# Kernel tuning notes

Hardware: AMD Instinct MI355X
Metric: run time of the kernel (lower is better)

Reference implementation:

```python
import jax, jax.numpy as jnp
import numpy as np

THETA0 = 3.0
THETA = 5.0
R = 5  # window radius == theta; the sdf is clipped to [-theta, theta], so distances beyond R are saturated

# all integer offsets within Euclidean radius THETA (78 of them)
_OFFSETS = [(dy, dx, float(np.hypot(dy, dx)))
            for dy in range(-R, R + 1) for dx in range(-R, R + 1)
            if np.hypot(dy, dx) <= THETA]


def _capped_edt(target_set):
    """target_set: bool [B,H,W]. Min Euclidean distance from each pixel to a True
    pixel, capped at THETA (exact for all values that survive the later clip)."""
    B, H, W = target_set.shape
    pad = jnp.pad(target_set, ((0, 0), (R, R), (R, R)), constant_values=False)
    d = jnp.full((B, H, W), THETA, dtype=jnp.float32)
    for dy, dx, dist in _OFFSETS:
        win = pad[:, R + dy:R + dy + H, R + dx:R + dx + W]
        d = jnp.minimum(d, jnp.where(win, jnp.float32(dist), jnp.float32(THETA)))
    return d


def _compute_sdf(mask):
    """mask: float [B,H,W]. Mirrors BoundaryLoss.compute_sdf:
    sdf_pos = edt(1-mask) = dist to nearest pixel where mask==1 (zeros of 1-mask)
    sdf_neg = edt(mask)   = dist to nearest pixel where mask==0
    (the `boundary` tensor in the torch code is computed but never used)."""
    sdf_pos = _capped_edt(mask == 1.0)
    sdf_neg = _capped_edt(mask == 0.0)
    sdf = jnp.clip(sdf_pos - sdf_neg, -THETA, THETA) / THETA
    empty = jnp.sum(mask, axis=(1, 2)) == 0.0  # per-batch empty-mask branch -> theta0
    return jnp.where(empty[:, None, None], jnp.float32(THETA0), sdf)


def _boundary_loss(pred, target):
    p = jax.nn.softmax(pred, axis=1)  # [B,C,H,W]
    C = pred.shape[1]
    loss = jnp.float32(0.0)
    for c in range(C):  # small fixed class count
        pred_sdf = _compute_sdf(p[:, c])
        tgt_sdf = _compute_sdf((target == c).astype(jnp.float32))
        loss = loss + jnp.mean(jnp.abs(pred_sdf - tgt_sdf))  # F.l1_loss, mean
    return loss / C


def setup_inputs() -> dict:
    key = jax.random.key(0)
    k1, k2 = jax.random.split(key)
    pred = jax.random.normal(k1, (16, 4, 512, 512), dtype=jnp.float32)
    target = jax.random.randint(k2, (16, 512, 512), 0, 4, dtype=jnp.int32)
    return {"pred": pred, "target": target}


def reference(pred, target):
    return _boundary_loss(pred, target)
```

## Files before the change

kernel.cpp:

```cpp
#include <hip/hip_runtime.h>
#include <stdint.h>

#define BB 16
#define CC 4
#define HH 512
#define WW 512
#define NWORDS 8
#define HW (HH * WW)

#define OFF_ROW   1024
#define OFF_TGT   262144
#define BOARD_BYTES (CC * BB * HH * NWORDS * 8)

__global__ void build_bits(const int* __restrict__ tgt,
                           const float* __restrict__ pred,
                           uint64_t* __restrict__ tgtb,
                           uint64_t* __restrict__ ppos,
                           uint64_t* __restrict__ pneg,
                           unsigned* __restrict__ rowsum,
                           float* __restrict__ out) {
    __shared__ unsigned srow[CC][8];
    int row = blockIdx.x;
    int b = row >> 9, y = row & (HH - 1);
    int x = threadIdx.x;
    if (row == 0 && x == 0) out[0] = 0.0f;

    int t = tgt[((size_t)(b * HH + y)) * WW + x];
    size_t i0 = (((size_t)b * CC) * HH + y) * (size_t)WW + x;
    float a0 = pred[i0];
    float a1 = pred[i0 + (size_t)HW];
    float a2 = pred[i0 + 2 * (size_t)HW];
    float a3 = pred[i0 + 3 * (size_t)HW];
    float m = fmaxf(fmaxf(a0, a1), fmaxf(a2, a3));
    float e0 = expf(a0 - m), e1 = expf(a1 - m), e2 = expf(a2 - m), e3 = expf(a3 - m);
    float s = (e0 + e1) + (e2 + e3);
    float p0 = e0 / s, p1 = e1 / s, p2 = e2 / s, p3 = e3 / s;

    int wv = x >> 6;
    bool l0 = (x & 63) == 0;
#define EMIT(cidx, pv)                                                        \
    {                                                                         \
        uint64_t mt = __ballot(t == (cidx));                                  \
        uint64_t mp = __ballot((pv) == 1.0f);                                 \
        uint64_t mn = __ballot((pv) == 0.0f);                                 \
        if (l0) {                                                             \
            size_t o = (((size_t)(cidx) * BB + b) * HH + y) * NWORDS + wv;    \
            tgtb[o] = mt;                                                     \
            ppos[o] = mp;                                                     \
            pneg[o] = mn;                                                     \
            srow[cidx][wv] = (mt != 0ull ? 1u : 0u) | (mp != 0ull ? 2u : 0u)  \
                           | (mn != 0ull ? 4u : 0u) | (mn == ~0ull ? 8u : 0u);\
        }                                                                     \
    }
    EMIT(0, p0)
    EMIT(1, p1)
    EMIT(2, p2)
    EMIT(3, p3)
#undef EMIT
    __syncthreads();
    if (x < CC) {
        unsigned o = 0u, a = 8u;
#pragma unroll
        for (int i = 0; i < 8; ++i) { o |= srow[x][i]; a &= srow[x][i]; }
        rowsum[((size_t)x * BB + b) * HH + y] = (o & 7u) | a;
    }
}

__device__ __forceinline__ constexpr int lev_idx(int d2) {
    return d2==0?0: d2==1?1: d2==2?2: d2==4?3: d2==5?4: d2==8?5: d2==9?6:
           d2==10?7: d2==13?8: d2==16?9: d2==17?10: d2==18?11: d2==20?12: 13;
}

__device__ __forceinline__ unsigned win11(const uint64_t* row10, int idx, int p) {
    uint64_t w;
    if (p < 64) {
        w = (row10[idx] >> p) | (row10[idx + 1] << (64 - p));
    } else {
        int q = p - 64;
        uint64_t M = row10[idx + 1];
        w = q ? ((M >> q) | (row10[idx + 2] << (64 - q))) : M;
    }
    return (unsigned)w & 0x7FFu;
}

__device__ __forceinline__ void upd(int& mind2, unsigned wbits, int dy2) {
    if (wbits) {
        unsigned hi = wbits >> 5;
        unsigned lo = wbits & 31u;
        int mdx = 6;
        if (hi) mdx = __ffs(hi) - 1;
        if (lo) {
            int m2 = 5 - (31 - __clz(lo));
            mdx = min(mdx, m2);
        }
        int cand = dy2 + mdx * mdx;
        mind2 = min(mind2, cand);
    }
}

__launch_bounds__(512)
__global__ void edt_main(const uint64_t* __restrict__ tgtb,
                         const uint64_t* __restrict__ pposb,
                         const uint64_t* __restrict__ pnegb,
                         const unsigned* __restrict__ rowsum,
                         float* __restrict__ out) {
    __shared__ uint64_t shm[74 * 8];
    __shared__ float wsum[8];
    __shared__ unsigned sflag[8];
    int tile = blockIdx.x & 7;
    int cb   = blockIdx.x >> 3;
    int y0   = tile * 64;
    const float INV_N = 1.0f / 16777216.0f;

    {
        unsigned rs = rowsum[(size_t)cb * HH + threadIdx.x];
        uint64_t bT = __ballot((rs & 1u) != 0u);
        uint64_t bP = __ballot((rs & 2u) != 0u);
        uint64_t bN = __ballot((rs & 4u) != 0u);
        uint64_t bAllNot = __ballot((rs & 8u) == 0u);
        if ((threadIdx.x & 63) == 0)
            sflag[threadIdx.x >> 6] = (bT ? 1u : 0u) | (bP ? 2u : 0u)
                                    | (bN ? 4u : 0u) | (bAllNot ? 8u : 0u);
        __syncthreads();
        if (threadIdx.x == 0) {
            unsigned o = 0u;
#pragma unroll
            for (int i = 0; i < 8; ++i) o |= sflag[i];
            sflag[0] = o;
        }
        __syncthreads();
    }
    unsigned F = sflag[0];
    bool present  = (F & 1u) != 0u;
    bool anyppos  = (F & 2u) != 0u;
    bool anypneg  = (F & 4u) != 0u;
    bool prednz   = (F & 8u) != 0u;
    bool fast     = !anyppos && !anypneg;
    __syncthreads();

    if (fast) {
        if (!present) {
            if (tile == 0 && threadIdx.x == 0)
                atomicAdd(out, 3.0f * (float)HW * INV_N);
            return;
        }
        uint64_t (*sT)[8] = (uint64_t (*)[8])shm;
        const uint64_t* board = tgtb + (size_t)cb * HH * NWORDS;
        for (int t = threadIdx.x; t < 74 * 8; t += 512) {
            int r = t >> 3, w = t & 7;
            int yy = y0 + r - 5;
            sT[r][w] = (yy >= 0 && yy < HH) ? board[(size_t)yy * NWORDS + w] : 0ull;
        }
        __syncthreads();

        int tr = threadIdx.x >> 3;
        int w  = threadIdx.x & 7;
        int y  = y0 + tr;

        uint64_t DT[14], DC[14];
#pragma unroll
        for (int k = 0; k < 14; ++k) { DT[k] = 0ull; DC[k] = 0ull; }

#pragma unroll
        for (int dy = -5; dy <= 5; ++dy) {
            int yy = y + dy;
            if (yy < 0 || yy >= HH) continue;
            const int ady  = dy < 0 ? -dy : dy;
            const int maxs = (ady == 0) ? 5 : (ady <= 3) ? 4 : (ady == 4) ? 3 : 0;
            int ly = tr + 5 + dy;
            uint64_t Cw = sT[ly][w];
            uint64_t Lw = (w > 0) ? sT[ly][w - 1] : 0ull;
            uint64_t Rw = (w < 7) ? sT[ly][w + 1] : 0ull;
            uint64_t Cc = ~Cw;
            uint64_t Lc = (w > 0) ? ~Lw : 0ull;
            uint64_t Rc = (w < 7) ? ~Rw : 0ull;
            uint64_t UT = Cw, UC = Cc;
            DT[lev_idx(ady * ady)] |= UT;
            DC[lev_idx(ady * ady)] |= UC;
#pragma unroll
            for (int s = 1; s <= 5; ++s) {
                if (s > maxs) break;
                UT |= (Cw >> s) | (Rw << (64 - s)) | (Cw << s) | (Lw >> (64 - s));
                UC |= (Cc >> s) | (Rc << (64 - s)) | (Cc << s) | (Lc >> (64 - s));
                const int li = lev_idx(ady * ady + s * s);
                DT[li] |= UT;
                DC[li] |= UC;
            }
        }

        const float dist[14] = {0.f, 1.f, 1.41421356f, 2.f, 2.23606798f,
            2.82842712f, 3.f, 3.16227766f, 3.60555128f, 4.f, 4.12310563f,
            4.24264069f, 4.47213595f, 5.f};
        uint64_t covT = 0ull, covC = 0ull;
        float s = 0.f;
#pragma unroll
        for (int k = 0; k < 14; ++k) {
            uint64_t nT = DT[k] & ~covT;
            uint64_t nC = DC[k] & ~covC;
            s += dist[k] * (float)(__popcll(nT) + __popcll(nC));
            covT |= DT[k];
            covC |= DC[k];
        }
        s += 5.f * (float)(__popcll(~covT) + __popcll(~covC));

        for (int o = 32; o > 0; o >>= 1) s += __shfl_down(s, o, 64);
        if ((threadIdx.x & 63) == 0) wsum[threadIdx.x >> 6] = s;
        __syncthreads();
        if (threadIdx.x == 0) {
            float tot = 0.f;
#pragma unroll
            for (int i = 0; i < 8; ++i) tot += wsum[i];
            atomicAdd(out, tot * 0.2f * INV_N);
        }
        return;
    }

    uint64_t (*sh)[11][10] = (uint64_t (*)[11][10])shm;
    int x = threadIdx.x;
    int idx = x >> 6, off = x & 63, p = off + 59;
    int b = cb & (BB - 1);
    int c = cb >> 4;

    unsigned vmask = 0x7FFu;
    if (x < 5) vmask &= (0x7FFu << (5 - x)) & 0x7FFu;
    if (x > WW - 6) vmask &= 0x7FFu >> (x - (WW - 6));

    float vsum = 0.f;
    for (int yy = 0; yy < 64; ++yy) {
        int y = y0 + yy;
        __syncthreads();
        for (int t = threadIdx.x; t < 330; t += 512) {
            int m = t / 110;
            int rem = t - m * 110;
            int r = rem / 10;
            int wi = rem - r * 10;
            int rowy = y + r - 5;
            uint64_t v = 0;
            if (wi >= 1 && wi <= 8 && rowy >= 0 && rowy < HH) {
                const uint64_t* src = (m == 0) ? tgtb : (m == 1) ? pposb : pnegb;
                v = src[(((size_t)c * BB + b) * HH + rowy) * NWORDS + (wi - 1)];
            }
            sh[m][r][wi] = v;
        }
        __syncthreads();

        int tp = 26, tn = 26, qp = 26, qn = 26;
#pragma unroll
        for (int dy = -5; dy <= 5; ++dy) {
            int ady = dy < 0 ? -dy : dy;
            unsigned allowed = (ady == 0) ? 0x7FFu
                             : (ady <= 3) ? 0x3FEu
                             : (ady == 4) ? 0x1FCu
                                          : 0x020u;
            int dy2 = dy * dy;
            int r = dy + 5;
            unsigned wt  = win11(&sh[0][r][0], idx, p);
            unsigned wpp = win11(&sh[1][r][0], idx, p);
            unsigned wpn = win11(&sh[2][r][0], idx, p);
            upd(tp, wt & allowed, dy2);
            upd(tn, (~wt) & vmask & allowed, dy2);
            upd(qp, wpp & allowed, dy2);
            upd(qn, wpn & allowed, dy2);
        }

        float dtp = (tp <= 25) ? sqrtf((float)tp) : 5.0f;
        float dtn = (tn <= 25) ? sqrtf((float)tn) : 5.0f;
        float dqp = (qp <= 25) ? sqrtf((float)qp) : 5.0f;
        float dqn = (qn <= 25) ? sqrtf((float)qn) : 5.0f;

        float td = fminf(fmaxf(dtp - dtn, -5.0f), 5.0f) / 5.0f;
        float qd = fminf(fmaxf(dqp - dqn, -5.0f), 5.0f) / 5.0f;
        float tsdf = present ? td : 3.0f;
        float psdf = prednz ? qd : 3.0f;
        vsum += fabsf(psdf - tsdf);
    }

    for (int o2 = 32; o2 > 0; o2 >>= 1) vsum += __shfl_down(vsum, o2, 64);
    if (off == 0) wsum[idx] = vsum;
    __syncthreads();
    if (threadIdx.x == 0) {
        float s = 0.f;
#pragma unroll
        for (int i = 0; i < 8; ++i) s += wsum[i];
        atomicAdd(out, s * INV_N);
    }
}

extern "C" void kernel_launch(void* const* d_in, const int* in_sizes, int n_in,
                              void* d_out, int out_size, void* d_ws, size_t ws_size,
                              hipStream_t stream) {
    const float* pred  = (const float*)d_in[0];
    const int* target  = (const int*)d_in[1];
    float* out = (float*)d_out;

    char* ws = (char*)d_ws;
    unsigned* rowsum = (unsigned*)(ws + OFF_ROW);
    uint64_t* tgtb   = (uint64_t*)(ws + OFF_TGT);
    uint64_t* pposb  = (uint64_t*)(ws + OFF_TGT + (size_t)BOARD_BYTES);
    uint64_t* pnegb  = (uint64_t*)(ws + OFF_TGT + 2 * (size_t)BOARD_BYTES);

    hipLaunchKernelGGL(build_bits, dim3(BB * HH), dim3(512), 0, stream,
                       target, pred, tgtb, pposb, pnegb, rowsum, out);
    hipLaunchKernelGGL(edt_main, dim3(CC * BB * 8), dim3(512), 0, stream,
                       tgtb, pposb, pnegb, rowsum, out);
}
```

Before: 125.4 us.

## Vectorize bit-board build, skip softmax when no saturation possible, trim EDT radius

The build kernel now processes four rows per block with int4/float4 loads, packs per-class bits via shuffles into 16-bit stores, and skips the exp/divide softmax entirely for a wavefront unless some pixel's logit range reaches 15, where a probability could round to exactly 0 or 1. Per-row flags for all four classes are packed into one word, replacing the per-class rowsum array. In the fast EDT path, the radius-5 level is dropped and the halo shrinks to 4 rows, using a hand-unrolled per-dy table, because uncovered pixels already default to distance 5. The logit-range threshold is a conservative numerical argument rather than an exact test, which is the main correctness risk.

```diff
diff --git a/kernel.cpp b/kernel.cpp
--- a/kernel.cpp
+++ b/kernel.cpp
@@ -12,63 +12,107 @@
 #define OFF_TGT   262144
 #define BOARD_BYTES (CC * BB * HH * NWORDS * 8)
 
+__launch_bounds__(512)
 __global__ void build_bits(const int* __restrict__ tgt,
                            const float* __restrict__ pred,
                            uint64_t* __restrict__ tgtb,
                            uint64_t* __restrict__ ppos,
                            uint64_t* __restrict__ pneg,
-                           unsigned* __restrict__ rowsum,
+                           unsigned* __restrict__ flags32,
                            float* __restrict__ out) {
-    __shared__ unsigned srow[CC][8];
-    int row = blockIdx.x;
+    __shared__ unsigned sfl[4][2];
+    int t = threadIdx.x;
+    int r = t >> 7;
+    int j = t & 127;
+    int row = blockIdx.x * 4 + r;
     int b = row >> 9, y = row & (HH - 1);
-    int x = threadIdx.x;
-    if (row == 0 && x == 0) out[0] = 0.0f;
-
-    int t = tgt[((size_t)(b * HH + y)) * WW + x];
-    size_t i0 = (((size_t)b * CC) * HH + y) * (size_t)WW + x;
-    float a0 = pred[i0];
-    float a1 = pred[i0 + (size_t)HW];
-    float a2 = pred[i0 + 2 * (size_t)HW];
-    float a3 = pred[i0 + 3 * (size_t)HW];
-    float m = fmaxf(fmaxf(a0, a1), fmaxf(a2, a3));
-    float e0 = expf(a0 - m), e1 = expf(a1 - m), e2 = expf(a2 - m), e3 = expf(a3 - m);
-    float s = (e0 + e1) + (e2 + e3);
-    float p0 = e0 / s, p1 = e1 / s, p2 = e2 / s, p3 = e3 / s;
-
-    int wv = x >> 6;
-    bool l0 = (x & 63) == 0;
-#define EMIT(cidx, pv)                                                        \
-    {                                                                         \
-        uint64_t mt = __ballot(t == (cidx));                                  \
-        uint64_t mp = __ballot((pv) == 1.0f);                                 \
-        uint64_t mn = __ballot((pv) == 0.0f);                                 \
-        if (l0) {                                                             \
-            size_t o = (((size_t)(cidx) * BB + b) * HH + y) * NWORDS + wv;    \
-            tgtb[o] = mt;                                                     \
-            ppos[o] = mp;                                                     \
-            pneg[o] = mn;                                                     \
-            srow[cidx][wv] = (mt != 0ull ? 1u : 0u) | (mp != 0ull ? 2u : 0u)  \
-                           | (mn != 0ull ? 4u : 0u) | (mn == ~0ull ? 8u : 0u);\
-        }                                                                     \
-    }
-    EMIT(0, p0)
-    EMIT(1, p1)
-    EMIT(2, p2)
-    EMIT(3, p3)
-#undef EMIT
+    if (blockIdx.x == 0 && t == 0) out[0] = 0.0f;
+
+    const int4* tg4 = reinterpret_cast<const int4*>(tgt);
+    int4 tv = tg4[(size_t)row * 128 + j];
+
+    float pa[4][4];
+    const float4* pr4 = reinterpret_cast<const float4*>(pred);
+#pragma unroll
+    for (int c = 0; c < 4; ++c) {
+        float4 v = pr4[((size_t)(b * 4 + c) * HH + y) * 128 + j];
+        pa[c][0] = v.x; pa[c][1] = v.y; pa[c][2] = v.z; pa[c][3] = v.w;
+    }
+
+    bool anyhard = false;
+#pragma unroll
+    for (int k = 0; k < 4; ++k) {
+        float mx = fmaxf(fmaxf(pa[0][k], pa[1][k]), fmaxf(pa[2][k], pa[3][k]));
+        float mn = fminf(fminf(pa[0][k], pa[1][k]), fminf(pa[2][k], pa[3][k]));
+        anyhard |= (mx - mn >= 15.0f);
+    }
+    uint64_t hard = __ballot(anyhard);
+
+    unsigned tn[4], ppn[4] = {0u, 0u, 0u, 0u}, pnn[4] = {0u, 0u, 0u, 0u};
+#pragma unroll
+    for (int c = 0; c < 4; ++c)
+        tn[c] = (unsigned)(tv.x == c) | ((unsigned)(tv.y == c) << 1)
+              | ((unsigned)(tv.z == c) << 2) | ((unsigned)(tv.w == c) << 3);
+
+    if (hard) {
+#pragma unroll
+        for (int k = 0; k < 4; ++k) {
+            float mx = fmaxf(fmaxf(pa[0][k], pa[1][k]), fmaxf(pa[2][k], pa[3][k]));
+            float e[4], s = 0.f;
+#pragma unroll
+            for (int c = 0; c < 4; ++c) { e[c] = expf(pa[c][k] - mx); s += e[c]; }
+#pragma unroll
+            for (int c = 0; c < 4; ++c) {
+                float p = e[c] / s;
+                ppn[c] |= (unsigned)(p == 1.0f) << k;
+                pnn[c] |= (unsigned)(p == 0.0f) << k;
+            }
+        }
+    }
+
+    unsigned fl = 0u;
+#pragma unroll
+    for (int c = 0; c < 4; ++c) {
+        unsigned f = (tn[c] ? 1u : 0u) | (ppn[c] ? 2u : 0u) | (pnn[c] ? 4u : 0u)
+                   | ((pnn[c] != 0xFu) ? 8u : 0u);
+        fl |= f << (4 * c);
+    }
+#pragma unroll
+    for (int o = 1; o < 64; o <<= 1) fl |= __shfl_xor(fl, o, 64);
+    if ((t & 63) == 0) sfl[r][(t >> 6) & 1] = fl;
+
+    unsigned short* t16 = reinterpret_cast<unsigned short*>(tgtb);
+    unsigned short* p16 = reinterpret_cast<unsigned short*>(ppos);
+    unsigned short* n16 = reinterpret_cast<unsigned short*>(pneg);
+#pragma unroll
+    for (int c = 0; c < 4; ++c) {
+        size_t base16 = ((size_t)(c * BB + b) * HH + y) * (NWORDS * 4);
+        unsigned v = tn[c];
+        v |= __shfl_down(v, 1, 64) << 4;
+        v |= __shfl_down(v, 2, 64) << 8;
+        if ((j & 3) == 0) t16[base16 + (j >> 2)] = (unsigned short)v;
+        if (hard) {
+            unsigned vp = ppn[c];
+            vp |= __shfl_down(vp, 1, 64) << 4;
+            vp |= __shfl_down(vp, 2, 64) << 8;
+            unsigned vn = pnn[c];
+            vn |= __shfl_down(vn, 1, 64) << 4;
+            vn |= __shfl_down(vn, 2, 64) << 8;
+            if ((j & 3) == 0) {
+                p16[base16 + (j >> 2)] = (unsigned short)vp;
+                n16[base16 + (j >> 2)] = (unsigned short)vn;
+            }
+        } else if ((j & 15) == 0) {
+            size_t wbase = ((size_t)(c * BB + b) * HH + y) * NWORDS + (j >> 4);
+            ppos[wbase] = 0ull;
+            pneg[wbase] = 0ull;
+        }
+    }
     __syncthreads();
-    if (x < CC) {
-        unsigned o = 0u, a = 8u;
-#pragma unroll
-        for (int i = 0; i < 8; ++i) { o |= srow[x][i]; a &= srow[x][i]; }
-        rowsum[((size_t)x * BB + b) * HH + y] = (o & 7u) | a;
-    }
-}
-
-__device__ __forceinline__ constexpr int lev_idx(int d2) {
-    return d2==0?0: d2==1?1: d2==2?2: d2==4?3: d2==5?4: d2==8?5: d2==9?6:
-           d2==10?7: d2==13?8: d2==16?9: d2==17?10: d2==18?11: d2==20?12: 13;
+    if (t < 4) {
+        int rr = blockIdx.x * 4 + t;
+        flags32[rr] = sfl[t][0] | sfl[t][1];
+    }
 }
 
 __device__ __forceinline__ unsigned win11(const uint64_t* row10, int idx, int p) {
@@ -98,29 +142,56 @@
     }
 }
 
+#define SSTEP(S, LI)                                                          \
+    UT |= (Cw >> (S)) | (Rw << (64 - (S))) | (Cw << (S)) | (Lw >> (64 - (S)));\
+    UC |= (Cc >> (S)) | (Rc << (64 - (S))) | (Cc << (S)) | (Lc >> (64 - (S)));\
+    DT[LI] |= UT; DC[LI] |= UC;
+
+#define PROW(DY, MAXS, LI0, LI1, LI2, LI3, LI4)                               \
+    do {                                                                      \
+        int yy = y + (DY);                                                    \
+        if (yy >= 0 && yy < HH) {                                             \
+            const int ly = tr + 4 + (DY);                                     \
+            uint64_t Cw = sT[ly][w];                                          \
+            uint64_t Lw = (w > 0) ? sT[ly][w - 1] : 0ull;                     \
+            uint64_t Rw = (w < 7) ? sT[ly][w + 1] : 0ull;                     \
+            uint64_t Cc = ~Cw;                                                \
+            uint64_t Lc = (w > 0) ? ~Lw : 0ull;                               \
+            uint64_t Rc = (w < 7) ? ~Rw : 0ull;                               \
+            uint64_t UT = Cw, UC = Cc;                                        \
+            DT[LI0] |= UT; DC[LI0] |= UC;                                     \
+            if ((MAXS) >= 1) { SSTEP(1, LI1) }                                \
+            if ((MAXS) >= 2) { SSTEP(2, LI2) }                                \
+            if ((MAXS) >= 3) { SSTEP(3, LI3) }                                \
+            if ((MAXS) >= 4) { SSTEP(4, LI4) }                                \
+        }                                                                     \
+    } while (0)
+
 __launch_bounds__(512)
 __global__ void edt_main(const uint64_t* __restrict__ tgtb,
                          const uint64_t* __restrict__ pposb,
                          const uint64_t* __restrict__ pnegb,
-                         const unsigned* __restrict__ rowsum,
+                         const unsigned* __restrict__ flags32,
                          float* __restrict__ out) {
-    __shared__ uint64_t shm[74 * 8];
+    __shared__ uint64_t shm[72 * 8];
     __shared__ float wsum[8];
     __shared__ unsigned sflag[8];
     int tile = blockIdx.x & 7;
     int cb   = blockIdx.x >> 3;
     int y0   = tile * 64;
+    int b = cb & (BB - 1);
+    int c = cb >> 4;
     const float INV_N = 1.0f / 16777216.0f;
 
     {
-        unsigned rs = rowsum[(size_t)cb * HH + threadIdx.x];
+        unsigned rs = (flags32[(size_t)b * HH + threadIdx.x] >> (4 * c)) & 0xFu;
         uint64_t bT = __ballot((rs & 1u) != 0u);
         uint64_t bP = __ballot((rs & 2u) != 0u);
         uint64_t bN = __ballot((rs & 4u) != 0u);
-        uint64_t bAllNot = __ballot((rs & 8u) == 0u);
+        uint64_t bZ = __ballot((rs & 8u) != 0u);
         if ((threadIdx.x & 63) == 0)
             sflag[threadIdx.x >> 6] = (bT ? 1u : 0u) | (bP ? 2u : 0u)
-                                    | (bN ? 4u : 0u) | (bAllNot ? 8u : 0u);
+                                    | (bN ? 4u : 0u) | (bZ ? 8u : 0u);
         __syncthreads();
         if (threadIdx.x == 0) {
             unsigned o = 0u;
@@ -136,7 +207,6 @@
     bool anypneg  = (F & 4u) != 0u;
     bool prednz   = (F & 8u) != 0u;
     bool fast     = !anyppos && !anypneg;
-    __syncthreads();
 
     if (fast) {
         if (!present) {
@@ -146,10 +216,10 @@
         }
         uint64_t (*sT)[8] = (uint64_t (*)[8])shm;
         const uint64_t* board = tgtb + (size_t)cb * HH * NWORDS;
-        for (int t = threadIdx.x; t < 74 * 8; t += 512) {
-            int r = t >> 3, w = t & 7;
-            int yy = y0 + r - 5;
-            sT[r][w] = (yy >= 0 && yy < HH) ? board[(size_t)yy * NWORDS + w] : 0ull;
+        for (int tt = threadIdx.x; tt < 72 * 8; tt += 512) {
+            int rr = tt >> 3, ww = tt & 7;
+            int yy = y0 + rr - 4;
+            sT[rr][ww] = (yy >= 0 && yy < HH) ? board[(size_t)yy * NWORDS + ww] : 0ull;
         }
         __syncthreads();
 
@@ -157,47 +227,30 @@
         int w  = threadIdx.x & 7;
         int y  = y0 + tr;
 
-        uint64_t DT[14], DC[14];
-#pragma unroll
-        for (int k = 0; k < 14; ++k) { DT[k] = 0ull; DC[k] = 0ull; }
-
-#pragma unroll
-        for (int dy = -5; dy <= 5; ++dy) {
-            int yy = y + dy;
-            if (yy < 0 || yy >= HH) continue;
-            const int ady  = dy < 0 ? -dy : dy;
-            const int maxs = (ady == 0) ? 5 : (ady <= 3) ? 4 : (ady == 4) ? 3 : 0;
-            int ly = tr + 5 + dy;
-            uint64_t Cw = sT[ly][w];
-            uint64_t Lw = (w > 0) ? sT[ly][w - 1] : 0ull;
-            uint64_t Rw = (w < 7) ? sT[ly][w + 1] : 0ull;
-            uint64_t Cc = ~Cw;
-            uint64_t Lc = (w > 0) ? ~Lw : 0ull;
-            uint64_t Rc = (w < 7) ? ~Rw : 0ull;
-            uint64_t UT = Cw, UC = Cc;
-            DT[lev_idx(ady * ady)] |= UT;
-            DC[lev_idx(ady * ady)] |= UC;
-#pragma unroll
-            for (int s = 1; s <= 5; ++s) {
-                if (s > maxs) break;
-                UT |= (Cw >> s) | (Rw << (64 - s)) | (Cw << s) | (Lw >> (64 - s));
-                UC |= (Cc >> s) | (Rc << (64 - s)) | (Cc << s) | (Lc >> (64 - s));
-                const int li = lev_idx(ady * ady + s * s);
-                DT[li] |= UT;
-                DC[li] |= UC;
-            }
-        }
-
-        const float dist[14] = {0.f, 1.f, 1.41421356f, 2.f, 2.23606798f,
+        uint64_t DT[13], DC[13];
+#pragma unroll
+        for (int k = 0; k < 13; ++k) { DT[k] = 0ull; DC[k] = 0ull; }
+
+        PROW(-4, 2,   9,  10,  12,   0,   0);
+        PROW(-3, 3,   6,   7,   8,  11,   0);
+        PROW(-2, 4,   3,   4,   5,   8,  12);
+        PROW(-1, 4,   1,   2,   4,   7,  10);
+        PROW( 0, 4,   0,   1,   3,   6,   9);
+        PROW( 1, 4,   1,   2,   4,   7,  10);
+        PROW( 2, 4,   3,   4,   5,   8,  12);
+        PROW( 3, 3,   6,   7,   8,  11,   0);
+        PROW( 4, 2,   9,  10,  12,   0,   0);
+
+        const float dist13[13] = {0.f, 1.f, 1.41421356f, 2.f, 2.23606798f,
             2.82842712f, 3.f, 3.16227766f, 3.60555128f, 4.f, 4.12310563f,
-            4.24264069f, 4.47213595f, 5.f};
-        uint64_t covT = 0ull, covC = 0ull;
+            4.24264069f, 4.47213595f};
+        uint64_t covT = DT[0], covC = DC[0];
         float s = 0.f;
 #pragma unroll
-        for (int k = 0; k < 14; ++k) {
+        for (int k = 1; k < 13; ++k) {
             uint64_t nT = DT[k] & ~covT;
             uint64_t nC = DC[k] & ~covC;
-            s += dist[k] * (float)(__popcll(nT) + __popcll(nC));
+            s += dist13[k] * (float)(__popcll(nT) + __popcll(nC));
             covT |= DT[k];
             covC |= DC[k];
         }
@@ -218,8 +271,6 @@
     uint64_t (*sh)[11][10] = (uint64_t (*)[11][10])shm;
     int x = threadIdx.x;
     int idx = x >> 6, off = x & 63, p = off + 59;
-    int b = cb & (BB - 1);
-    int c = cb >> 4;
 
     unsigned vmask = 0x7FFu;
     if (x < 5) vmask &= (0x7FFu << (5 - x)) & 0x7FFu;
@@ -229,18 +280,18 @@
     for (int yy = 0; yy < 64; ++yy) {
         int y = y0 + yy;
         __syncthreads();
-        for (int t = threadIdx.x; t < 330; t += 512) {
-            int m = t / 110;
-            int rem = t - m * 110;
-            int r = rem / 10;
-            int wi = rem - r * 10;
-            int rowy = y + r - 5;
+        for (int tt = threadIdx.x; tt < 330; tt += 512) {
+            int m = tt / 110;
+            int rem = tt - m * 110;
+            int rr = rem / 10;
+            int wi = rem - rr * 10;
+            int rowy = y + rr - 5;
             uint64_t v = 0;
             if (wi >= 1 && wi <= 8 && rowy >= 0 && rowy < HH) {
                 const uint64_t* src = (m == 0) ? tgtb : (m == 1) ? pposb : pnegb;
                 v = src[(((size_t)c * BB + b) * HH + rowy) * NWORDS + (wi - 1)];
             }
-            sh[m][r][wi] = v;
+            sh[m][rr][wi] = v;
         }
         __syncthreads();
 
@@ -253,10 +304,10 @@
                              : (ady == 4) ? 0x1FCu
                                           : 0x020u;
             int dy2 = dy * dy;
-            int r = dy + 5;
-            unsigned wt  = win11(&sh[0][r][0], idx, p);
-            unsigned wpp = win11(&sh[1][r][0], idx, p);
-            unsigned wpn = win11(&sh[2][r][0], idx, p);
+            int rr = dy + 5;
+            unsigned wt  = win11(&sh[0][rr][0], idx, p);
+            unsigned wpp = win11(&sh[1][rr][0], idx, p);
+            unsigned wpn = win11(&sh[2][rr][0], idx, p);
             upd(tp, wt & allowed, dy2);
             upd(tn, (~wt) & vmask & allowed, dy2);
             upd(qp, wpp & allowed, dy2);
@@ -279,10 +330,10 @@
     if (off == 0) wsum[idx] = vsum;
     __syncthreads();
     if (threadIdx.x == 0) {
-        float s = 0.f;
-#pragma unroll
-        for (int i = 0; i < 8; ++i) s += wsum[i];
-        atomicAdd(out, s * INV_N);
+        float stot = 0.f;
+#pragma unroll
+        for (int i = 0; i < 8; ++i) stot += wsum[i];
+        atomicAdd(out, stot * INV_N);
     }
 }
 
@@ -294,13 +345,13 @@
     float* out = (float*)d_out;
 
     char* ws = (char*)d_ws;
-    unsigned* rowsum = (unsigned*)(ws + OFF_ROW);
-    uint64_t* tgtb   = (uint64_t*)(ws + OFF_TGT);
-    uint64_t* pposb  = (uint64_t*)(ws + OFF_TGT + (size_t)BOARD_BYTES);
-    uint64_t* pnegb  = (uint64_t*)(ws + OFF_TGT + 2 * (size_t)BOARD_BYTES);
-
-    hipLaunchKernelGGL(build_bits, dim3(BB * HH), dim3(512), 0, stream,
-                       target, pred, tgtb, pposb, pnegb, rowsum, out);
+    unsigned* flags32 = (unsigned*)(ws + OFF_ROW);
+    uint64_t* tgtb    = (uint64_t*)(ws + OFF_TGT);
+    uint64_t* pposb   = (uint64_t*)(ws + OFF_TGT + (size_t)BOARD_BYTES);
+    uint64_t* pnegb   = (uint64_t*)(ws + OFF_TGT + 2 * (size_t)BOARD_BYTES);
+
+    hipLaunchKernelGGL(build_bits, dim3(BB * HH / 4), dim3(512), 0, stream,
+                       target, pred, tgtb, pposb, pnegb, flags32, out);
     hipLaunchKernelGGL(edt_main, dim3(CC * BB * 8), dim3(512), 0, stream,
-                       tgtb, pposb, pnegb, rowsum, out);
-}
+                       tgtb, pposb, pnegb, flags32, out);
+}
```

Measured after the change: 112.1 us. 10.6% less time.
